# Kernel tuning notes

Hardware: AMD Instinct MI355X
Metric: run time of the kernel (lower is better)

The kernel has to match this reference:

```python
import jax, jax.numpy as jnp
import numpy as np

BLANK = 0          # tf.nn.ctc_loss default blank_index (StringLookup reserves 0 for OOV)
PAD = 127          # padding_value = char_to_num.vocabulary_size()
NEG = -1e30        # log-space 'zero' (avoid -inf to keep grads NaN-free)
B, T, C, L = 1024, 256, 128, 32


def setup_inputs() -> dict:
    key = jax.random.key(0)
    k1, k2 = jax.random.split(key)
    # labels in [1, PAD-1]; none equal PAD so label_length == L (full-length labels)
    y_true = jax.random.randint(k1, (B, L), 1, PAD).astype(jnp.int32)
    y_pred = jax.random.normal(k2, (B, T, C), dtype=jnp.float32)
    return {"y_true": y_true, "y_pred": y_pred}


def _ctc_loss(y_true, y_pred):
    """Faithful jax version of tf.nn.ctc_loss(labels, logits, label_len, T,
    logits_time_major=False, blank_index=0): standard log-space alpha DP."""
    Bn, Tn, Cn = y_pred.shape
    Ln = y_true.shape[1]
    S = 2 * Ln + 1  # extended label length (blanks interleaved)

    logp = jax.nn.log_softmax(y_pred, axis=-1)                    # [B,T,C]

    # extended label sequence: blank, l1, blank, l2, ..., blank   # [B,S]
    ext = jnp.full((Bn, S), BLANK, dtype=y_true.dtype)
    ext = ext.at[:, 1::2].set(y_true)

    # log-probs gathered at extended-label symbols                # [B,T,S]
    lp_ext = jnp.take_along_axis(
        logp, jnp.broadcast_to(ext[:, None, :], (Bn, Tn, S)), axis=2)

    # label_length = count of non-padding entries (mirrors count_nonzero)
    label_len = jnp.sum(y_true != PAD, axis=1)                    # [B]

    # skip transition s-2 -> s allowed iff ext[s] is a non-blank differing
    # from ext[s-2]
    skip_ok = jnp.concatenate(
        [jnp.zeros((Bn, 2), bool),
         (ext[:, 2:] != BLANK) & (ext[:, 2:] != ext[:, :-2])], axis=1)  # [B,S]

    neg1 = jnp.full((Bn, 1), NEG, logp.dtype)
    neg2 = jnp.full((Bn, 2), NEG, logp.dtype)

    alpha0 = jnp.full((Bn, S), NEG, logp.dtype)
    alpha0 = alpha0.at[:, 0].set(lp_ext[:, 0, 0]).at[:, 1].set(lp_ext[:, 0, 1])

    def step(alpha, lp_t):  # alpha,[B,S]  lp_t,[B,S]
        a1 = jnp.concatenate([neg1, alpha[:, :-1]], axis=1)
        a2 = jnp.concatenate([neg2, alpha[:, :-2]], axis=1)
        a2 = jnp.where(skip_ok, a2, NEG)
        new = lp_t + jnp.logaddexp(jnp.logaddexp(alpha, a1), a2)
        return new, None

    lp_seq = jnp.transpose(lp_ext, (1, 0, 2))                     # [T,B,S]
    alphaT, _ = jax.lax.scan(step, alpha0, lp_seq[1:])            # [B,S]

    # total log-likelihood ends at last blank (2*len) or last label (2*len-1)
    bi = jnp.arange(Bn)
    e1 = 2 * label_len
    e2 = 2 * label_len - 1
    loglik = jnp.logaddexp(alphaT[bi, e1], alphaT[bi, e2])        # [B]
    return -loglik


def reference(y_true, y_pred):
    # The original layer returns y_pred and registers the loss via add_loss;
    # the compute-dominant quantity is the per-example CTC loss, returned here.
    return _ctc_loss(y_true, y_pred)
```

## Files before the change

kernel.cpp:

```cpp
#include <hip/hip_runtime.h>
#include <cstdint>


#define CTC_BLANK 0
#define CTC_PAD   127
#define NEG       (-1e30f)
#define LOG2E     1.44269504088896340736f
#define LN2       0.69314718055994530942f

constexpr int Bn = 1024, Tn = 256, Cn = 128, Ln = 32;
constexpr int NSLOT = Ln + 1;
constexpr int CR  = 16;
constexpr int NCH = Tn / CR;
constexpr int CF  = CR * Cn;

__device__ __forceinline__ float fexp2(float x) { return __builtin_amdgcn_exp2f(x); }
__device__ __forceinline__ float flog2(float x) { return __builtin_amdgcn_logf(x); }

template <int CTRL>
__device__ __forceinline__ float dpp_add(float s) {
    int v = __builtin_amdgcn_update_dpp(0, __float_as_int(s), CTRL, 0xF, 0xF, true);
    return s + __int_as_float(v);
}
__device__ __forceinline__ float dpp_wave_shr1(float src, float old) {
    return __int_as_float(__builtin_amdgcn_update_dpp(
        __float_as_int(old), __float_as_int(src), 0x138, 0xF, 0xF, false));
}
__device__ __forceinline__ void gl_lds16(const float* g, float* l) {
    __builtin_amdgcn_global_load_lds(
        (const __attribute__((address_space(1))) uint32_t*)g,
        (__attribute__((address_space(3))) uint32_t*)l, 16, 0, 0);
}

__global__ __launch_bounds__(512, 8) void ctc_fused_kernel(
        const int*   __restrict__ y_true,
        const float* __restrict__ y_pred,
        float*       __restrict__ out)
{
    __shared__ __align__(16) float raw[2][CF];
    __shared__ _Float16 Gc[Tn * NSLOT];
    __shared__ int   labels[Ln];
    __shared__ __align__(16) int cmap[Cn];
    __shared__ int   used[Cn];
    __shared__ int   wcnt[8];
    __shared__ float partS[16];

    const int b    = blockIdx.x;
    const int tid  = threadIdx.x;
    const int lane = tid & 63;
    const int wave = tid >> 6;

    const float* gbase = y_pred + (size_t)b * Tn * Cn;

    auto stage = [&](int c, int buf) {
        gl_lds16(gbase + c * CF + tid * 4, &raw[buf][wave * 256]);
    };

    stage(0, 0);

    if (tid < Ln) labels[tid] = y_true[b * Ln + tid];
    if (tid < Cn) used[tid] = 0;
    __syncthreads();
    if (tid == 0) used[CTC_BLANK] = 1;
    if (tid < Ln) used[labels[tid]] = 1;
    __syncthreads();
    {
        bool f = (tid < Cn) && (used[tid] != 0);
        unsigned long long m = __ballot(f);
        if (lane == 0) wcnt[wave] = __popcll(m);
        __syncthreads();
        int base = 0;
        for (int w = 0; w < wave; ++w) base += wcnt[w];
        if (tid < Cn)
            cmap[tid] = f ? (base + __popcll(m & ((1ull << lane) - 1ull))) : -1;
        __syncthreads();
    }

    const int half = lane >> 5;
    const int l32  = lane & 31;
    const int4 cm  = ((const int4*)cmap)[l32];
    float acc = 0.f;

    const int  i      = lane;
    const bool validO = (i < Ln);
    const bool validE = (i <= Ln);
    const int  myLab   = validO ? labels[i] : -1;
    const int  prevLab = (i >= 1 && i < Ln) ? labels[i - 1] : -1;
    const int  slotO   = validO ? cmap[myLab] : 0;
    const bool skipO   = (i >= 1 && i < Ln) &&
                         (myLab != CTC_BLANK) && (myLab != prevLab);
    const int  len = __popcll(__ballot(validO && (myLab != CTC_PAD)));
    float aE = NEG, aO = NEG;

    auto dp_chunk = [&](int t0, int t1) {
        int t = t0;
        if (t == 0) {
            aE = (i == 0) ? (float)Gc[0]     : NEG;
            aO = (i == 0) ? (float)Gc[slotO] : NEG;
            t = 1;
        }
        float pB[2], pO[2];
        const int ta = t, tb = (t + 1 < t1) ? t + 1 : t1 - 1;
        pB[0] = (float)Gc[ta * NSLOT]; pO[0] = (float)Gc[ta * NSLOT + slotO];
        pB[1] = (float)Gc[tb * NSLOT]; pO[1] = (float)Gc[tb * NSLOT + slotO];
        int k = 0;
        #pragma unroll 2
        for (; t < t1; ++t) {
            const float lpB = pB[k], lpO = pO[k];
            const int tp = (t + 2 < t1) ? t + 2 : t1 - 1;
            pB[k] = (float)Gc[tp * NSLOT];
            pO[k] = (float)Gc[tp * NSLOT + slotO];
            k ^= 1;

            const float aOup = dpp_wave_shr1(aO, NEG);
            const float m  = fmaxf(aE, aOup);
            const float e1 = fexp2(aE - m);
            const float e2 = fexp2(aOup - m);
            const float sE = e1 + e2;
            const float nE = lpB + m + flog2(sE);
            const float m3 = fmaxf(aO, m);
            const float nO = lpO + m3 +
                flog2(fexp2(aO - m3) + (skipO ? sE : e1) * fexp2(m - m3));
            aE = validE ? nE : NEG;
            aO = validO ? nO : NEG;
        }
    };

    for (int c = 0; c < NCH; ++c) {
        if (c + 1 < NCH) stage(c + 1, (c + 1) & 1);

        {
            const int rl = 2 * wave + half;
            const int r  = c * CR + rl;
            const float4 x = ((const float4*)&raw[c & 1][rl * Cn])[l32];
            if (cm.x >= 0) Gc[r * NSLOT + cm.x] = (_Float16)(x.x * LOG2E);
            if (cm.y >= 0) Gc[r * NSLOT + cm.y] = (_Float16)(x.y * LOG2E);
            if (cm.z >= 0) Gc[r * NSLOT + cm.z] = (_Float16)(x.z * LOG2E);
            if (cm.w >= 0) Gc[r * NSLOT + cm.w] = (_Float16)(x.w * LOG2E);
            float s = __expf(x.x) + __expf(x.y) + __expf(x.z) + __expf(x.w);
            s = dpp_add<0x111>(s);
            s = dpp_add<0x112>(s);
            s = dpp_add<0x114>(s);
            s = dpp_add<0x118>(s);
            s = dpp_add<0x142>(s);
            acc += __logf(s);
        }

        if (wave == 0 && c > 0) dp_chunk((c - 1) * CR, c * CR);
        if (c == NCH - 1 && l32 == 31) partS[wave * 2 + half] = acc;
        __syncthreads();
    }

    if (wave == 0) {
        dp_chunk(Tn - CR, Tn);
        const float v1 = __shfl(aE, len, 64);
        const float v2 = __shfl(aO, len - 1, 64);
        if (i == 0) {
            float S = 0.f;
            #pragma unroll
            for (int j = 0; j < 16; ++j) S += partS[j];
            const float mm = fmaxf(v1, v2);
            const float L2 = mm + flog2(fexp2(v1 - mm) + fexp2(v2 - mm));
            out[b] = S - LN2 * L2;
        }
    }
}

extern "C" void kernel_launch(void* const* d_in, const int* in_sizes, int n_in,
                              void* d_out, int out_size, void* d_ws, size_t ws_size,
                              hipStream_t stream) {
    const int*   y_true = (const int*)d_in[0];
    const float* y_pred = (const float*)d_in[1];
    float*       out    = (float*)d_out;
    ctc_fused_kernel<<<Bn, 512, 0, stream>>>(y_true, y_pred, out);
}
```

Before: 206.7 us.

## Give each wave private staging buffers and run the CTC DP after staging

Each wave now streams its own two rows per chunk into a private double-buffered LDS region. This removes the block-wide barrier that was needed after every chunk. The alpha recursion is no longer interleaved chunk-by-chunk with staging; wave 0 runs all time steps in one loop after a single barrier. The intent is to cut barrier overhead and let the loader waves finish early. The cost is losing the overlap between the serial DP and the data loading inside a block, and correctness now depends on the compiler inserting waits for the async LDS loads.

Result: slower. 222.6 us (+7.7%).

```diff
diff --git a/kernel.cpp b/kernel.cpp
--- a/kernel.cpp
+++ b/kernel.cpp
@@ -12,7 +12,6 @@
 constexpr int NSLOT = Ln + 1;
 constexpr int CR  = 16;
 constexpr int NCH = Tn / CR;
-constexpr int CF  = CR * Cn;
 
 __device__ __forceinline__ float fexp2(float x) { return __builtin_amdgcn_exp2f(x); }
 __device__ __forceinline__ float flog2(float x) { return __builtin_amdgcn_logf(x); }
@@ -37,7 +36,7 @@
         const float* __restrict__ y_pred,
         float*       __restrict__ out)
 {
-    __shared__ __align__(16) float raw[2][CF];
+    __shared__ __align__(16) float raw[8][2][CR / 8 * Cn];
     __shared__ _Float16 Gc[Tn * NSLOT];
     __shared__ int   labels[Ln];
     __shared__ __align__(16) int cmap[Cn];
@@ -53,7 +52,8 @@
     const float* gbase = y_pred + (size_t)b * Tn * Cn;
 
     auto stage = [&](int c, int buf) {
-        gl_lds16(gbase + c * CF + tid * 4, &raw[buf][wave * 256]);
+        const float* g = gbase + (size_t)(c * CR + 2 * wave) * Cn + lane * 4;
+        gl_lds16(g, &raw[wave][buf][0]);
     };
 
     stage(0, 0);
@@ -81,33 +81,48 @@
     const int4 cm  = ((const int4*)cmap)[l32];
     float acc = 0.f;
 
-    const int  i      = lane;
-    const bool validO = (i < Ln);
-    const bool validE = (i <= Ln);
-    const int  myLab   = validO ? labels[i] : -1;
-    const int  prevLab = (i >= 1 && i < Ln) ? labels[i - 1] : -1;
-    const int  slotO   = validO ? cmap[myLab] : 0;
-    const bool skipO   = (i >= 1 && i < Ln) &&
-                         (myLab != CTC_BLANK) && (myLab != prevLab);
-    const int  len = __popcll(__ballot(validO && (myLab != CTC_PAD)));
-    float aE = NEG, aO = NEG;
+    for (int c = 0; c < NCH; ++c) {
+        const float4 x = ((const float4*)&raw[wave][c & 1][0])[lane];
+        if (c + 1 < NCH) stage(c + 1, (c + 1) & 1);
 
-    auto dp_chunk = [&](int t0, int t1) {
-        int t = t0;
-        if (t == 0) {
-            aE = (i == 0) ? (float)Gc[0]     : NEG;
-            aO = (i == 0) ? (float)Gc[slotO] : NEG;
-            t = 1;
-        }
+        const int r = c * CR + 2 * wave + half;
+        if (cm.x >= 0) Gc[r * NSLOT + cm.x] = (_Float16)(x.x * LOG2E);
+        if (cm.y >= 0) Gc[r * NSLOT + cm.y] = (_Float16)(x.y * LOG2E);
+        if (cm.z >= 0) Gc[r * NSLOT + cm.z] = (_Float16)(x.z * LOG2E);
+        if (cm.w >= 0) Gc[r * NSLOT + cm.w] = (_Float16)(x.w * LOG2E);
+        float s = __expf(x.x) + __expf(x.y) + __expf(x.z) + __expf(x.w);
+        s = dpp_add<0x111>(s);
+        s = dpp_add<0x112>(s);
+        s = dpp_add<0x114>(s);
+        s = dpp_add<0x118>(s);
+        s = dpp_add<0x142>(s);
+        acc += __logf(s);
+    }
+    if (l32 == 31) partS[wave * 2 + half] = acc;
+    __syncthreads();
+
+    if (wave == 0) {
+        const int  i      = lane;
+        const bool validO = (i < Ln);
+        const bool validE = (i <= Ln);
+        const int  myLab   = validO ? labels[i] : -1;
+        const int  prevLab = (i >= 1 && i < Ln) ? labels[i - 1] : -1;
+        const int  slotO   = validO ? cmap[myLab] : 0;
+        const bool skipO   = (i >= 1 && i < Ln) &&
+                             (myLab != CTC_BLANK) && (myLab != prevLab);
+        const int  len = __popcll(__ballot(validO && (myLab != CTC_PAD)));
+
+        float aE = (i == 0) ? (float)Gc[0]     : NEG;
+        float aO = (i == 0) ? (float)Gc[slotO] : NEG;
+
         float pB[2], pO[2];
-        const int ta = t, tb = (t + 1 < t1) ? t + 1 : t1 - 1;
-        pB[0] = (float)Gc[ta * NSLOT]; pO[0] = (float)Gc[ta * NSLOT + slotO];
-        pB[1] = (float)Gc[tb * NSLOT]; pO[1] = (float)Gc[tb * NSLOT + slotO];
+        pB[0] = (float)Gc[NSLOT];     pO[0] = (float)Gc[NSLOT + slotO];
+        pB[1] = (float)Gc[2 * NSLOT]; pO[1] = (float)Gc[2 * NSLOT + slotO];
         int k = 0;
         #pragma unroll 2
-        for (; t < t1; ++t) {
+        for (int t = 1; t < Tn; ++t) {
             const float lpB = pB[k], lpO = pO[k];
-            const int tp = (t + 2 < t1) ? t + 2 : t1 - 1;
+            const int tp = (t + 2 < Tn) ? t + 2 : Tn - 1;
             pB[k] = (float)Gc[tp * NSLOT];
             pO[k] = (float)Gc[tp * NSLOT + slotO];
             k ^= 1;
@@ -124,35 +139,7 @@
             aE = validE ? nE : NEG;
             aO = validO ? nO : NEG;
         }
-    };
 
-    for (int c = 0; c < NCH; ++c) {
-        if (c + 1 < NCH) stage(c + 1, (c + 1) & 1);
-
-        {
-            const int rl = 2 * wave + half;
-            const int r  = c * CR + rl;
-            const float4 x = ((const float4*)&raw[c & 1][rl * Cn])[l32];
-            if (cm.x >= 0) Gc[r * NSLOT + cm.x] = (_Float16)(x.x * LOG2E);
-            if (cm.y >= 0) Gc[r * NSLOT + cm.y] = (_Float16)(x.y * LOG2E);
-            if (cm.z >= 0) Gc[r * NSLOT + cm.z] = (_Float16)(x.z * LOG2E);
-            if (cm.w >= 0) Gc[r * NSLOT + cm.w] = (_Float16)(x.w * LOG2E);
-            float s = __expf(x.x) + __expf(x.y) + __expf(x.z) + __expf(x.w);
-            s = dpp_add<0x111>(s);
-            s = dpp_add<0x112>(s);
-            s = dpp_add<0x114>(s);
-            s = dpp_add<0x118>(s);
-            s = dpp_add<0x142>(s);
-            acc += __logf(s);
-        }
-
-        if (wave == 0 && c > 0) dp_chunk((c - 1) * CR, c * CR);
-        if (c == NCH - 1 && l32 == 31) partS[wave * 2 + half] = acc;
-        __syncthreads();
-    }
-
-    if (wave == 0) {
-        dp_chunk(Tn - CR, Tn);
         const float v1 = __shfl(aE, len, 64);
         const float v2 = __shfl(aO, len - 1, 64);
         if (i == 0) {
```
